# Optimization experiments

Hardware: AMD Instinct MI355X
Metric: run time of the kernel (lower is better)

The kernel has to match this reference:

```python
import jax, jax.numpy as jnp
import numpy as np

CH_IN = 256
CH_OUT = 32


def setup_inputs() -> dict:
    key = jax.random.key(0)
    ks = jax.random.split(key, 7)
    b, c, H, W = 4, CH_IN, 64, 64
    x = jax.random.normal(ks[0], (b, c, H, W), dtype=jnp.float32)
    # 1x1 conv weights (out, in) and biases, small init like torch default
    sc_in = 1.0 / np.sqrt(CH_IN)
    Wf = jax.random.uniform(ks[1], (CH_OUT, CH_IN), jnp.float32, -sc_in, sc_in)
    bf = jax.random.uniform(ks[2], (CH_OUT,), jnp.float32, -sc_in, sc_in)
    Wg = jax.random.uniform(ks[3], (CH_OUT, CH_IN), jnp.float32, -sc_in, sc_in)
    bg = jax.random.uniform(ks[4], (CH_OUT,), jnp.float32, -sc_in, sc_in)
    Wh = jax.random.uniform(ks[5], (CH_IN, CH_IN), jnp.float32, -sc_in, sc_in)
    bh = jax.random.uniform(ks[6], (CH_IN,), jnp.float32, -sc_in, sc_in)
    return {"x": x, "Wf": Wf, "bf": bf, "Wg": Wg, "bg": bg, "Wh": Wh, "bh": bh}


def reference(x, Wf, bf, Wg, bg, Wh, bh):
    b, c, H, W = x.shape
    xf = x.reshape(b, c, H * W)                      # [b, c, N]
    # 1x1 convs == per-pixel linear projections
    f = jnp.einsum('oc,bcn->bon', Wf, xf) + bf[None, :, None]   # [b, ch_out, N]
    g = jnp.einsum('oc,bcn->bon', Wg, xf) + bg[None, :, None]   # [b, ch_out, N]
    h = jnp.einsum('oc,bcn->bon', Wh, xf) + bh[None, :, None]   # [b, ch_in, N]
    # s[b, i, j] = sum_o f[b,o,i] * g[b,o,j]
    s = jnp.einsum('boi,boj->bij', f, g)             # [b, N, N]
    # torch softmax over dim=1 (the i axis)
    beta = jax.nn.softmax(s, axis=1)                 # [b, N, N]
    # o = h @ beta : [b, c, N] x [b, N, N] -> [b, c, N]
    o = jnp.einsum('bcn,bnm->bcm', h, beta)
    return o.reshape(b, c, H, W)
```

## Files before the change

kernel.cpp:

```cpp
#include <hip/hip_runtime.h>
#include <hip/hip_bf16.h>
#include <math.h>

#define BATCH 4
#define CIN   256
#define DQK   32
#define NPIX  4096
#define MTOT  320

typedef __attribute__((ext_vector_type(4))) float f32x4;
typedef __attribute__((ext_vector_type(8))) short bf16x8;
typedef __attribute__((ext_vector_type(4))) unsigned int u32x4;

__device__ __forceinline__ unsigned short f2bf(float f) {
  unsigned u = __builtin_bit_cast(unsigned, f);
  u += 0x7FFFu + ((u >> 16) & 1u);
  return (unsigned short)(u >> 16);
}
__device__ __forceinline__ unsigned pk2(float a, float b) {
  return (unsigned)f2bf(a) | ((unsigned)f2bf(b) << 16);
}
__device__ __forceinline__ void barrier_lds() {
  asm volatile("s_waitcnt lgkmcnt(0)" ::: "memory");
  __builtin_amdgcn_s_barrier();
  asm volatile("" ::: "memory");
}

__global__ void wcvt(const float* __restrict__ Wh, const float* __restrict__ Wf,
                     const float* __restrict__ Wg,
                     const float* __restrict__ bh, const float* __restrict__ bf,
                     const float* __restrict__ bg,
                     unsigned short* __restrict__ Wb, float* __restrict__ bcat) {
  const int r = blockIdx.x;
  const int c = threadIdx.x;
  const float* src = (r < 256) ? &Wh[r * CIN] : (r < 288) ? &Wf[(r - 256) * CIN] : &Wg[(r - 288) * CIN];
  Wb[r * CIN + c] = f2bf(src[c]);
  if (c == 0)
    bcat[r] = (r < 256) ? bh[r] : (r < 288) ? bf[r - 256] : bg[r - 288];
}

#define XPAD 4
__launch_bounds__(512, 1)
__global__ void proj_all(const float* __restrict__ x, const unsigned short* __restrict__ Wb,
                         const float* __restrict__ bcat,
                         unsigned short* __restrict__ F, unsigned short* __restrict__ G,
                         unsigned short* __restrict__ H) {
  __shared__ unsigned short Xs[64 * (CIN + XPAD)];

  const int bid = blockIdx.x;
  const int b = bid >> 6;
  const int n0 = (bid & 63) << 6;
  const int t = threadIdx.x;
  const int lane = t & 63;
  const int w = t >> 6;

  const float* __restrict__ xb = x + (size_t)b * CIN * NPIX + n0;
#pragma unroll
  for (int p = 0; p < 16; ++p) {
    const int k = p * 16 + w * 2;
    const float a0 = xb[(size_t)k * NPIX + lane];
    const float a1 = xb[(size_t)(k + 1) * NPIX + lane];
    const unsigned pk = (unsigned)f2bf(a0) | ((unsigned)f2bf(a1) << 16);
    *(unsigned*)((char*)Xs + lane * (CIN + XPAD) * 2 + k * 2) = pk;
  }
  __syncthreads();

  const int l16 = lane & 15, lhi = lane >> 4;
  const int wm = w >> 1;
  const int wn = w & 1;

  const f32x4 fzero = {0.f, 0.f, 0.f, 0.f};
  f32x4 acc[5][2];
#pragma unroll
  for (int i = 0; i < 5; ++i)
#pragma unroll
    for (int j = 0; j < 2; ++j) acc[i][j] = fzero;

#pragma unroll
  for (int ks = 0; ks < 8; ++ks) {
    bf16x8 bx[2];
#pragma unroll
    for (int j = 0; j < 2; ++j)
      bx[j] = *(const bf16x8*)&Xs[(wn * 32 + j * 16 + l16) * (CIN + XPAD) + ks * 32 + lhi * 8];
#pragma unroll
    for (int i = 0; i < 5; ++i) {
      const bf16x8 aw = *(const bf16x8*)(Wb + (size_t)(wm * 80 + i * 16 + l16) * CIN + ks * 32 + lhi * 8);
#pragma unroll
      for (int j = 0; j < 2; ++j)
        acc[i][j] = __builtin_amdgcn_mfma_f32_16x16x32_bf16(aw, bx[j], acc[i][j], 0, 0, 0);
    }
  }

#pragma unroll
  for (int i = 0; i < 5; ++i) {
    const int MT = wm * 5 + i;
    const int m0 = MT * 16;
    const f32x4 bias = *(const f32x4*)&bcat[m0 + lhi * 4];
#pragma unroll
    for (int j = 0; j < 2; ++j) {
      const int n = n0 + wn * 32 + j * 16 + l16;
      f32x4 v = acc[i][j];
      v.x += bias.x; v.y += bias.y; v.z += bias.z; v.w += bias.w;
      if (MT < 16) {
        const int c0 = m0 + lhi * 4;
        unsigned short* dst = H + ((size_t)b * CIN + c0) * NPIX + n;
        dst[0 * NPIX] = f2bf(v.x);
        dst[1 * NPIX] = f2bf(v.y);
        dst[2 * NPIX] = f2bf(v.z);
        dst[3 * NPIX] = f2bf(v.w);
      } else {
        unsigned short* dst = (MT < 18) ? F : G;
        const int d0 = ((MT - 16) & 1) * 16 + lhi * 4;
        uint2 pk;
        pk.x = (unsigned)f2bf(v.x) | ((unsigned)f2bf(v.y) << 16);
        pk.y = (unsigned)f2bf(v.z) | ((unsigned)f2bf(v.w) << 16);
        *(uint2*)(dst + ((size_t)b * NPIX + n) * DQK + d0) = pk;
      }
    }
  }
}

#define BNK  64
#define KEYS 2048
#define NTILE (KEYS / BNK)

__launch_bounds__(512, 2)
__global__ void attn_split(const unsigned short* __restrict__ F,
                           const unsigned short* __restrict__ G,
                           const unsigned short* __restrict__ H,
                           unsigned short* __restrict__ Ap, float* __restrict__ Lp) {
  __shared__ unsigned short Kl[2][64][40];
  __shared__ unsigned short Vl[2][256][72];
  __shared__ unsigned short Pl[2][2][64][72];

  const int bid = blockIdx.x;
  const int slab = bid & 7;
  const int b = slab >> 1;
  const int split = slab & 1;
  const int qt = bid >> 3;
  const int t = threadIdx.x;
  const int lane = t & 63, w = t >> 6;
  const int l16 = lane & 15, lhi = lane >> 4;
  const int mg = w >> 2, cs = w & 3;

  const unsigned short* Fb = F + (size_t)b * NPIX * DQK;
  const unsigned short* Gb = G + (size_t)b * NPIX * DQK;
  const unsigned short* Hb = H + (size_t)b * CIN * NPIX;
  const int nb0 = split * KEYS;
  const int q0 = qt * 128 + mg * 64;

  const f32x4 fzero = {0.f, 0.f, 0.f, 0.f};

  bf16x8 qf[4];
#pragma unroll
  for (int mt = 0; mt < 4; ++mt)
    qf[mt] = *(const bf16x8*)(Gb + (size_t)(q0 + mt * 16 + l16) * DQK + lhi * 8);

  f32x4 acc[4][4];
#pragma unroll
  for (int ct = 0; ct < 4; ++ct)
#pragma unroll
    for (int mt = 0; mt < 4; ++mt) acc[ct][mt] = fzero;
  float Lacc[4] = {0.f, 0.f, 0.f, 0.f};

  const int vrow = t >> 3, vslot = t & 7;
  const int krow = t >> 2, kslot = t & 3;
  const unsigned short* Vg = Hb + (size_t)vrow * NPIX + nb0 + vslot * 8;
  const unsigned short* Kg = Fb + (size_t)(nb0 + krow) * DQK + kslot * 8;

  u32x4 vr[4];
  u32x4 kr = {0, 0, 0, 0};

#define LOADT(TT) do {                                                          \
    _Pragma("unroll")                                                           \
    for (int i_ = 0; i_ < 4; ++i_)                                              \
      vr[i_] = *(const u32x4*)(Vg + (size_t)i_ * 64 * NPIX + (size_t)(TT) * BNK);\
    if (t < 256) kr = *(const u32x4*)(Kg + (size_t)(TT) * BNK * DQK);           \
  } while (0)

#define STORET(BUF) do {                                                        \
    _Pragma("unroll")                                                           \
    for (int i_ = 0; i_ < 4; ++i_)                                              \
      *(u32x4*)&Vl[BUF][i_ * 64 + vrow][vslot * 8] = vr[i_];                    \
    if (t < 256) *(u32x4*)&Kl[BUF][krow][kslot * 8] = kr;                       \
  } while (0)

#define QKSM(BUF, PAR) do {                                                     \
    const bf16x8 kf_ = *(const bf16x8*)&Kl[BUF][cs * 16 + l16][lhi * 8];        \
    f32x4 s_[4];                                                                \
    _Pragma("unroll")                                                           \
    for (int mt_ = 0; mt_ < 4; ++mt_)                                           \
      s_[mt_] = __builtin_amdgcn_mfma_f32_16x16x32_bf16(kf_, qf[mt_], fzero, 0, 0, 0); \
    _Pragma("unroll")                                                           \
    for (int mt_ = 0; mt_ < 4; ++mt_) {                                         \
      const float p0 = __expf(s_[mt_][0]), p1 = __expf(s_[mt_][1]);             \
      const float p2 = __expf(s_[mt_][2]), p3 = __expf(s_[mt_][3]);             \
      Lacc[mt_] += (p0 + p1) + (p2 + p3);                                       \
      uint2 pk_; pk_.x = pk2(p0, p1); pk_.y = pk2(p2, p3);                      \
      *(uint2*)&Pl[PAR][mg][mt_ * 16 + l16][cs * 16 + lhi * 4] = pk_;           \
    }                                                                           \
  } while (0)

  LOADT(0); STORET(0);
  LOADT(1); STORET(1);
  LOADT(2);
  barrier_lds();
  QKSM(0, 0);

  for (int tt = 0; tt < NTILE; ++tt) {
    const int buf = tt & 1;
    barrier_lds();
    bf16x8 pf[4][2];
#pragma unroll
    for (int mt = 0; mt < 4; ++mt)
#pragma unroll
      for (int kk = 0; kk < 2; ++kk)
        pf[mt][kk] = *(const bf16x8*)&Pl[buf][mg][mt * 16 + l16][kk * 32 + lhi * 8];
    if (tt + 1 < NTILE) QKSM(buf ^ 1, buf ^ 1);
    __builtin_amdgcn_s_setprio(1);
#pragma unroll
    for (int kk = 0; kk < 2; ++kk)
#pragma unroll
      for (int ct = 0; ct < 4; ++ct) {
        const bf16x8 vf = *(const bf16x8*)&Vl[buf][cs * 64 + ct * 16 + l16][kk * 32 + lhi * 8];
#pragma unroll
        for (int mt = 0; mt < 4; ++mt)
          acc[ct][mt] = __builtin_amdgcn_mfma_f32_16x16x32_bf16(vf, pf[mt][kk], acc[ct][mt], 0, 0, 0);
      }
    __builtin_amdgcn_s_setprio(0);
    barrier_lds();
    if (tt + 2 < NTILE) STORET(buf);
    if (tt + 3 < NTILE) LOADT(tt + 3);
  }
#undef LOADT
#undef STORET
#undef QKSM

#pragma unroll
  for (int mt = 0; mt < 4; ++mt) {
    float L = Lacc[mt];
    L += __shfl_xor(L, 16, 64);
    L += __shfl_xor(L, 32, 64);
    if (lhi == 0)
      Lp[((size_t)split * 4 + cs) * (4 * NPIX) + (size_t)b * NPIX + q0 + mt * 16 + l16] = L;
  }
#pragma unroll
  for (int ct = 0; ct < 4; ++ct)
#pragma unroll
    for (int mt = 0; mt < 4; ++mt) {
      const int c = cs * 64 + ct * 16 + lhi * 4;
      const int q = q0 + mt * 16 + l16;
      unsigned short* dst = Ap + (((size_t)split * 4 + b) * CIN + c) * NPIX + q;
#pragma unroll
      for (int v = 0; v < 4; ++v) dst[(size_t)v * NPIX] = f2bf(acc[ct][mt][v]);
    }
}

__global__ void combineL(const float* __restrict__ Lp, float* __restrict__ Linv) {
  const int idx = blockIdx.x * 256 + threadIdx.x;
  float s = 0.f;
#pragma unroll
  for (int i = 0; i < 8; ++i) s += Lp[(size_t)i * (4 * NPIX) + idx];
  Linv[idx] = 1.f / s;
}

__global__ void combine(const unsigned short* __restrict__ Ap, const float* __restrict__ Linv,
                        float* __restrict__ out) {
  const size_t base = ((size_t)blockIdx.x * 256 + threadIdx.x) * 8;
  const int b = (int)(base / ((size_t)CIN * NPIX));
  const int q = (int)(base % NPIX);
  const u32x4 a0 = *(const u32x4*)(Ap + base);
  const u32x4 a1 = *(const u32x4*)(Ap + (size_t)4 * CIN * NPIX + base);
  const float* lv = &Linv[(size_t)b * NPIX + q];
  float r[8];
#pragma unroll
  for (int i = 0; i < 4; ++i) {
    const float x0 = __builtin_bit_cast(float, (a0[i] & 0xFFFFu) << 16) +
                     __builtin_bit_cast(float, (a1[i] & 0xFFFFu) << 16);
    const float x1 = __builtin_bit_cast(float, (a0[i] & 0xFFFF0000u)) +
                     __builtin_bit_cast(float, (a1[i] & 0xFFFF0000u));
    r[2 * i] = x0 * lv[2 * i];
    r[2 * i + 1] = x1 * lv[2 * i + 1];
  }
  *(f32x4*)&out[base] = *(f32x4*)&r[0];
  *(f32x4*)&out[base + 4] = *(f32x4*)&r[4];
}

#define BN 32
__launch_bounds__(512, 2)
__global__ void attn_kernel(const unsigned short* __restrict__ F,
                            const unsigned short* __restrict__ G,
                            const unsigned short* __restrict__ H,
                            float* __restrict__ out) {
  __shared__ unsigned short Klds[32 * 40];
  __shared__ unsigned short Vlds[256 * 40];
  __shared__ unsigned short Plds[8][32 * 40];

  const int bid = blockIdx.x;
  const int b = bid >> 6;
  const int t = threadIdx.x;
  const int lane = t & 63;
  const int w = t >> 6;
  const int l16 = lane & 15;
  const int lhi = lane >> 4;
  const int m0 = ((bid & 63) << 6) + ((w >> 2) << 5);
  const int c0 = (w & 3) << 6;

  const f32x4 fzero = {0.f, 0.f, 0.f, 0.f};

  bf16x8 qf[2];
#pragma unroll
  for (int mt = 0; mt < 2; ++mt)
    qf[mt] = *(const bf16x8*)(G + ((size_t)b * NPIX + m0 + mt * 16 + l16) * DQK + lhi * 8);

  f32x4 acc[4][2];
#pragma unroll
  for (int ct = 0; ct < 4; ++ct)
#pragma unroll
    for (int mt = 0; mt < 2; ++mt) acc[ct][mt] = fzero;
  float Mr[2] = {-INFINITY, -INFINITY};
  float Lr[2] = {0.f, 0.f};

  const unsigned short* Fb = F + (size_t)b * NPIX * DQK;
  const unsigned short* Hb = H + (size_t)b * CIN * NPIX;
  unsigned short* Pw = &Plds[w][0];

  for (int n0 = 0; n0 < NPIX; n0 += BN) {
    __syncthreads();
    if (t < 128) {
      const int nr = t >> 2, sl = t & 3;
      *(u32x4*)&Klds[nr * 40 + sl * 8] = *(const u32x4*)(Fb + (size_t)(n0 + nr) * DQK + sl * 8);
    }
#pragma unroll
    for (int i = 0; i < 2; ++i) {
      const int q = t + i * 512;
      const int cr = q >> 2, sl = q & 3;
      *(u32x4*)&Vlds[cr * 40 + sl * 8] = *(const u32x4*)(Hb + (size_t)cr * NPIX + n0 + sl * 8);
    }
    __syncthreads();

    bf16x8 kf[2];
#pragma unroll
    for (int nts = 0; nts < 2; ++nts)
      kf[nts] = *(const bf16x8*)&Klds[(nts * 16 + l16) * 40 + lhi * 8];
    f32x4 s[2][2];
#pragma unroll
    for (int mt = 0; mt < 2; ++mt)
#pragma unroll
      for (int nts = 0; nts < 2; ++nts)
        s[mt][nts] = __builtin_amdgcn_mfma_f32_16x16x32_bf16(kf[nts], qf[mt], fzero, 0, 0, 0);

#pragma unroll
    for (int mt = 0; mt < 2; ++mt) {
      float tmax = s[mt][0][0];
#pragma unroll
      for (int v = 1; v < 4; ++v) tmax = fmaxf(tmax, s[mt][0][v]);
#pragma unroll
      for (int v = 0; v < 4; ++v) tmax = fmaxf(tmax, s[mt][1][v]);
      tmax = fmaxf(tmax, __shfl_xor(tmax, 16, 64));
      tmax = fmaxf(tmax, __shfl_xor(tmax, 32, 64));
      const float newM = fmaxf(Mr[mt], tmax);
      const float rescale = __expf(Mr[mt] - newM);
      Mr[mt] = newM;
      float p[2][4];
      float psum = 0.f;
#pragma unroll
      for (int nts = 0; nts < 2; ++nts)
#pragma unroll
        for (int v = 0; v < 4; ++v) {
          p[nts][v] = __expf(s[mt][nts][v] - newM);
          psum += p[nts][v];
        }
      psum += __shfl_xor(psum, 16, 64);
      psum += __shfl_xor(psum, 32, 64);
      Lr[mt] = Lr[mt] * rescale + psum;
#pragma unroll
      for (int ct = 0; ct < 4; ++ct) acc[ct][mt] *= rescale;
#pragma unroll
      for (int nts = 0; nts < 2; ++nts) {
        uint2 pkv;
        pkv.x = (unsigned)f2bf(p[nts][0]) | ((unsigned)f2bf(p[nts][1]) << 16);
        pkv.y = (unsigned)f2bf(p[nts][2]) | ((unsigned)f2bf(p[nts][3]) << 16);
        *(uint2*)&Pw[(mt * 16 + l16) * 40 + nts * 16 + lhi * 4] = pkv;
      }
    }
    asm volatile("" ::: "memory");

    bf16x8 pf[2];
#pragma unroll
    for (int mt = 0; mt < 2; ++mt)
      pf[mt] = *(const bf16x8*)&Pw[(mt * 16 + l16) * 40 + lhi * 8];
#pragma unroll
    for (int ct = 0; ct < 4; ++ct) {
      const bf16x8 vf = *(const bf16x8*)&Vlds[(c0 + ct * 16 + l16) * 40 + lhi * 8];
#pragma unroll
      for (int mt = 0; mt < 2; ++mt)
        acc[ct][mt] = __builtin_amdgcn_mfma_f32_16x16x32_bf16(vf, pf[mt], acc[ct][mt], 0, 0, 0);
    }
  }

#pragma unroll
  for (int mt = 0; mt < 2; ++mt) {
    const float invL = 1.f / Lr[mt];
    const int m = m0 + mt * 16 + l16;
#pragma unroll
    for (int ct = 0; ct < 4; ++ct)
#pragma unroll
      for (int v = 0; v < 4; ++v) {
        const int c = c0 + ct * 16 + lhi * 4 + v;
        out[((size_t)b * CIN + c) * NPIX + m] = acc[ct][mt][v] * invL;
      }
  }
}

extern "C" void kernel_launch(void* const* d_in, const int* in_sizes, int n_in,
                              void* d_out, int out_size, void* d_ws, size_t ws_size,
                              hipStream_t stream) {
  (void)in_sizes; (void)n_in; (void)out_size;
  const float* x  = (const float*)d_in[0];
  const float* Wf = (const float*)d_in[1];
  const float* bf = (const float*)d_in[2];
  const float* Wg = (const float*)d_in[3];
  const float* bg = (const float*)d_in[4];
  const float* Wh = (const float*)d_in[5];
  const float* bh = (const float*)d_in[6];
  float* out = (float*)d_out;

  unsigned short* Fw = (unsigned short*)d_ws;
  unsigned short* Gw = Fw + (size_t)BATCH * NPIX * DQK;
  unsigned short* Hw = Gw + (size_t)BATCH * NPIX * DQK;
  unsigned short* Wb = Hw + (size_t)BATCH * CIN * NPIX;
  float* bcat = (float*)(Wb + (size_t)MTOT * CIN);
  unsigned short* Apart = (unsigned short*)(bcat + MTOT);
  float* Lpart = (float*)(Apart + (size_t)2 * BATCH * CIN * NPIX);
  float* Linv  = Lpart + (size_t)8 * BATCH * NPIX;
  const size_t NEED = (size_t)((char*)(Linv + (size_t)BATCH * NPIX) - (char*)d_ws);

  hipLaunchKernelGGL(wcvt, dim3(MTOT), dim3(256), 0, stream, Wh, Wf, Wg, bh, bf, bg, Wb, bcat);
  hipLaunchKernelGGL(proj_all, dim3(BATCH * 64), dim3(512), 0, stream, x, Wb, bcat, Fw, Gw, Hw);

  if (ws_size >= NEED) {
    hipLaunchKernelGGL(attn_split, dim3(BATCH * 32 * 2), dim3(512), 0, stream, Fw, Gw, Hw, Apart, Lpart);
    hipLaunchKernelGGL(combineL, dim3(BATCH * NPIX / 256), dim3(256), 0, stream, Lpart, Linv);
    hipLaunchKernelGGL(combine, dim3((size_t)BATCH * CIN * NPIX / 8 / 256), dim3(256), 0, stream, Apart, Linv, out);
  } else {
    hipLaunchKernelGGL(attn_kernel, dim3(BATCH * 64), dim3(512), 0, stream, Fw, Gw, Hw, out);
  }
}
```

Baseline: 87.50 us.

## Load K/V tiles directly to LDS with global_load_lds and triple buffering

Replaces the register-staged global-to-LDS copies in the attention kernel with direct global_load_lds transfers into a three-deep ring of K/V buffers. The LDS layout drops its padding and uses an XOR swizzle to avoid bank conflicts. Partial vmcnt waits let loads stay in flight across iterations. The larger LDS footprint forces launch bounds down to one block per CU, which risks lower occupancy and less latency hiding.

```diff
diff --git a/kernel.cpp b/kernel.cpp
--- a/kernel.cpp
+++ b/kernel.cpp
@@ -25,6 +25,12 @@
   __builtin_amdgcn_s_barrier();
   asm volatile("" ::: "memory");
 }
+__device__ __forceinline__ void wait_vm4_lgkm0() { asm volatile("s_waitcnt vmcnt(4) lgkmcnt(0)" ::: "memory"); }
+__device__ __forceinline__ void wait_vm5_lgkm0() { asm volatile("s_waitcnt vmcnt(5) lgkmcnt(0)" ::: "memory"); }
+
+#define GLD16(GP, LP) \
+  __builtin_amdgcn_global_load_lds((const __attribute__((address_space(1))) void*)(GP), \
+                                   (__attribute__((address_space(3))) void*)(LP), 16, 0, 0)
 
 __global__ void wcvt(const float* __restrict__ Wh, const float* __restrict__ Wf,
                      const float* __restrict__ Wg,
@@ -124,13 +130,13 @@
 #define KEYS 2048
 #define NTILE (KEYS / BNK)
 
-__launch_bounds__(512, 2)
+__launch_bounds__(512, 1)
 __global__ void attn_split(const unsigned short* __restrict__ F,
                            const unsigned short* __restrict__ G,
                            const unsigned short* __restrict__ H,
                            unsigned short* __restrict__ Ap, float* __restrict__ Lp) {
-  __shared__ unsigned short Kl[2][64][40];
-  __shared__ unsigned short Vl[2][256][72];
+  __shared__ unsigned short Kl[3][64][32];
+  __shared__ unsigned short Vl[3][256][64];
   __shared__ unsigned short Pl[2][2][64][72];
 
   const int bid = blockIdx.x;
@@ -163,78 +169,83 @@
     for (int mt = 0; mt < 4; ++mt) acc[ct][mt] = fzero;
   float Lacc[4] = {0.f, 0.f, 0.f, 0.f};
 
-  const int vrow = t >> 3, vslot = t & 7;
-  const int krow = t >> 2, kslot = t & 3;
-  const unsigned short* Vg = Hb + (size_t)vrow * NPIX + nb0 + vslot * 8;
-  const unsigned short* Kg = Fb + (size_t)(nb0 + krow) * DQK + kslot * 8;
-
-  u32x4 vr[4];
-  u32x4 kr = {0, 0, 0, 0};
-
-#define LOADT(TT) do {                                                          \
-    _Pragma("unroll")                                                           \
-    for (int i_ = 0; i_ < 4; ++i_)                                              \
-      vr[i_] = *(const u32x4*)(Vg + (size_t)i_ * 64 * NPIX + (size_t)(TT) * BNK);\
-    if (t < 256) kr = *(const u32x4*)(Kg + (size_t)(TT) * BNK * DQK);           \
+  const char* vsrc = (const char*)Hb + ((size_t)(8 * w + (lane >> 3)) * NPIX + nb0) * 2
+                   + (((lane & 7) ^ (lane >> 3)) * 16);
+  const int kw = (w >= 4) ? (w - 4) : 0;
+  const char* ksrc = (const char*)Fb + ((size_t)(nb0 + 16 * kw + (lane >> 2)) * DQK) * 2
+                   + (((lane & 3) ^ ((lane >> 2) & 3)) * 16);
+
+#define ISSUE(TT) do {                                                           \
+    const int bu_ = (TT) % 3;                                                    \
+    _Pragma("unroll")                                                            \
+    for (int i_ = 0; i_ < 4; ++i_)                                               \
+      GLD16(vsrc + (size_t)i_ * 64 * NPIX * 2 + (size_t)(TT) * 128,              \
+            &Vl[bu_][i_ * 64 + 8 * w][0]);                                       \
+    if (w >= 4)                                                                  \
+      GLD16(ksrc + (size_t)(TT) * 64 * DQK * 2, &Kl[bu_][16 * kw][0]);           \
   } while (0)
 
-#define STORET(BUF) do {                                                        \
-    _Pragma("unroll")                                                           \
-    for (int i_ = 0; i_ < 4; ++i_)                                              \
-      *(u32x4*)&Vl[BUF][i_ * 64 + vrow][vslot * 8] = vr[i_];                    \
-    if (t < 256) *(u32x4*)&Kl[BUF][krow][kslot * 8] = kr;                       \
+#define BSTART() do {                                                            \
+    if (w >= 4) wait_vm5_lgkm0(); else wait_vm4_lgkm0();                         \
+    __builtin_amdgcn_s_barrier();                                                \
+    asm volatile("" ::: "memory");                                               \
   } while (0)
 
-#define QKSM(BUF, PAR) do {                                                     \
-    const bf16x8 kf_ = *(const bf16x8*)&Kl[BUF][cs * 16 + l16][lhi * 8];        \
-    f32x4 s_[4];                                                                \
-    _Pragma("unroll")                                                           \
-    for (int mt_ = 0; mt_ < 4; ++mt_)                                           \
+#define QKSM(BUF3, PAR) do {                                                     \
+    const unsigned short* kb_ = &Kl[BUF3][0][0];                                 \
+    const bf16x8 kf_ = *(const bf16x8*)(kb_ + (cs * 16 + l16) * 32 + ((lhi ^ (l16 & 3)) * 8)); \
+    f32x4 s_[4];                                                                 \
+    _Pragma("unroll")                                                            \
+    for (int mt_ = 0; mt_ < 4; ++mt_)                                            \
       s_[mt_] = __builtin_amdgcn_mfma_f32_16x16x32_bf16(kf_, qf[mt_], fzero, 0, 0, 0); \
-    _Pragma("unroll")                                                           \
-    for (int mt_ = 0; mt_ < 4; ++mt_) {                                         \
-      const float p0 = __expf(s_[mt_][0]), p1 = __expf(s_[mt_][1]);             \
-      const float p2 = __expf(s_[mt_][2]), p3 = __expf(s_[mt_][3]);             \
-      Lacc[mt_] += (p0 + p1) + (p2 + p3);                                       \
-      uint2 pk_; pk_.x = pk2(p0, p1); pk_.y = pk2(p2, p3);                      \
-      *(uint2*)&Pl[PAR][mg][mt_ * 16 + l16][cs * 16 + lhi * 4] = pk_;           \
-    }                                                                           \
+    _Pragma("unroll")                                                            \
+    for (int mt_ = 0; mt_ < 4; ++mt_) {                                          \
+      const float p0 = __expf(s_[mt_][0]), p1 = __expf(s_[mt_][1]);              \
+      const float p2 = __expf(s_[mt_][2]), p3 = __expf(s_[mt_][3]);              \
+      Lacc[mt_] += (p0 + p1) + (p2 + p3);                                        \
+      uint2 pk_; pk_.x = pk2(p0, p1); pk_.y = pk2(p2, p3);                       \
+      *(uint2*)&Pl[PAR][mg][mt_ * 16 + l16][cs * 16 + lhi * 4] = pk_;            \
+    }                                                                            \
   } while (0)
 
-  LOADT(0); STORET(0);
-  LOADT(1); STORET(1);
-  LOADT(2);
-  barrier_lds();
+#define PVACC(BUF3, PF) do {                                                     \
+    const unsigned short* vb_ = &Vl[BUF3][0][0];                                 \
+    __builtin_amdgcn_s_setprio(1);                                               \
+    _Pragma("unroll")                                                            \
+    for (int kk_ = 0; kk_ < 2; ++kk_)                                            \
+      _Pragma("unroll")                                                          \
+      for (int ct_ = 0; ct_ < 4; ++ct_) {                                        \
+        const bf16x8 vf_ = *(const bf16x8*)(vb_ + (cs * 64 + ct_ * 16 + l16) * 64 \
+                            + (((4 * kk_ + lhi) ^ (l16 & 7)) * 8));              \
+        _Pragma("unroll")                                                        \
+        for (int mt_ = 0; mt_ < 4; ++mt_)                                        \
+          acc[ct_][mt_] = __builtin_amdgcn_mfma_f32_16x16x32_bf16(vf_, PF[mt_][kk_], acc[ct_][mt_], 0, 0, 0); \
+      }                                                                          \
+    __builtin_amdgcn_s_setprio(0);                                               \
+  } while (0)
+
+  ISSUE(0); ISSUE(1); ISSUE(2);
+  BSTART();
   QKSM(0, 0);
 
   for (int tt = 0; tt < NTILE; ++tt) {
-    const int buf = tt & 1;
+    const int par = tt & 1;
+    BSTART();
+    bf16x8 pf[4][2];
+#pragma unroll
+    for (int mt = 0; mt < 4; ++mt)
+#pragma unroll
+      for (int kk = 0; kk < 2; ++kk)
+        pf[mt][kk] = *(const bf16x8*)&Pl[par][mg][mt * 16 + l16][kk * 32 + lhi * 8];
+    if (tt + 1 < NTILE) QKSM((tt + 1) % 3, par ^ 1);
+    PVACC(tt % 3, pf);
     barrier_lds();
-    bf16x8 pf[4][2];
-#pragma unroll
-    for (int mt = 0; mt < 4; ++mt)
-#pragma unroll
-      for (int kk = 0; kk < 2; ++kk)
-        pf[mt][kk] = *(const bf16x8*)&Pl[buf][mg][mt * 16 + l16][kk * 32 + lhi * 8];
-    if (tt + 1 < NTILE) QKSM(buf ^ 1, buf ^ 1);
-    __builtin_amdgcn_s_setprio(1);
-#pragma unroll
-    for (int kk = 0; kk < 2; ++kk)
-#pragma unroll
-      for (int ct = 0; ct < 4; ++ct) {
-        const bf16x8 vf = *(const bf16x8*)&Vl[buf][cs * 64 + ct * 16 + l16][kk * 32 + lhi * 8];
-#pragma unroll
-        for (int mt = 0; mt < 4; ++mt)
-          acc[ct][mt] = __builtin_amdgcn_mfma_f32_16x16x32_bf16(vf, pf[mt][kk], acc[ct][mt], 0, 0, 0);
-      }
-    __builtin_amdgcn_s_setprio(0);
-    barrier_lds();
-    if (tt + 2 < NTILE) STORET(buf);
-    if (tt + 3 < NTILE) LOADT(tt + 3);
-  }
-#undef LOADT
-#undef STORET
+    if (tt + 3 < NTILE) ISSUE(tt + 3);
+  }
+#undef ISSUE
+#undef BSTART
 #undef QKSM
+#undef PVACC
 
 #pragma unroll
   for (int mt = 0; mt < 4; ++mt) {
```

Result: no change. 87.99 us (+0.6%).
